# Optimization experiments

Hardware: AMD Instinct MI355X
Metric: run time of the kernel (lower is better)

The kernel has to match this reference:

```python
import jax, jax.numpy as jnp
import numpy as np
from jax import lax

TOP_K = 4
ROUTED_SCALING = 1.0
RENORMALIZE = True


def setup_inputs() -> dict:
    key = jax.random.key(0)
    ks = jax.random.split(key, 9)
    H, I, E = 2048, 1024, 16
    s = 0.02
    return {
        "hidden_states": jax.random.normal(ks[0], (2, 1024, H), jnp.float32),
        "gate_w": jax.random.normal(ks[1], (E, H), jnp.float32) * s,
        "expert_bias": jax.random.normal(ks[2], (E,), jnp.float32) * s,
        "w_gate": jax.random.normal(ks[3], (E, I, H), jnp.float32) * s,
        "w_up": jax.random.normal(ks[4], (E, I, H), jnp.float32) * s,
        "w_down": jax.random.normal(ks[5], (E, H, I), jnp.float32) * s,
        "sw_gate": jax.random.normal(ks[6], (I, H), jnp.float32) * s,
        "sw_up": jax.random.normal(ks[7], (I, H), jnp.float32) * s,
        "sw_down": jax.random.normal(ks[8], (H, I), jnp.float32) * s,
    }


def _swiglu_ffn(x, wg, wu, wd):
    # SiluAndMul(gate_up) -> down_proj
    return (jax.nn.silu(x @ wg.T) * (x @ wu.T)) @ wd.T


def reference(hidden_states, gate_w, expert_bias, w_gate, w_up, w_down,
              sw_gate, sw_up, sw_down):
    orig_shape = hidden_states.shape
    H = orig_shape[-1]
    x = hidden_states.reshape(-1, H)            # [T, H]
    T = x.shape[0]

    # --- sigmoid gating with score-correction bias (bias affects selection only) ---
    logits = x.astype(jnp.float32) @ gate_w.T    # [T, E] fp32 router
    scores = jax.nn.sigmoid(logits)
    _, topk_idx = lax.top_k(scores + expert_bias[None, :], TOP_K)   # [T, K]
    topk_w = jnp.take_along_axis(scores, topk_idx, axis=-1)         # raw scores
    if RENORMALIZE:
        topk_w = topk_w / jnp.sum(topk_w, axis=-1, keepdims=True)
    topk_w = topk_w * ROUTED_SCALING

    # scatter top-k weights into dense [T, E] combine matrix
    E = gate_w.shape[0]
    combine = jnp.zeros((T, E), dtype=x.dtype).at[
        jnp.arange(T)[:, None], topk_idx].set(topk_w.astype(x.dtype))

    # --- routed experts: scan over experts, weighted accumulate ---
    def step(acc, ws):
        wg, wu, wd, cw = ws                     # cw: [T] combine weights
        return acc + cw[:, None] * _swiglu_ffn(x, wg, wu, wd), None

    routed, _ = lax.scan(step, jnp.zeros_like(x),
                         (w_gate, w_up, w_down, combine.T))

    # --- shared expert ---
    shared = _swiglu_ffn(x, sw_gate, sw_up, sw_down)

    return (routed + shared).reshape(orig_shape)
```

## Files before the change

### kernel.cpp

```cpp
#include <hip/hip_runtime.h>
#include <hip/hip_bf16.h>
#include <cstdint>

#define TK 2048
#define HD 2048
#define ID 1024
#define NE 16
#define NG 17
#define TOPK 4
#define SLOTS (TK*TOPK)
#define ROWS_ALL (SLOTS+TK)
#define IH (ID*HD)
#define MAXT 96

typedef __attribute__((ext_vector_type(4))) float f32x4;
typedef __attribute__((ext_vector_type(8))) short s16x8;
typedef unsigned short u16;
typedef unsigned long long u64;

__device__ __forceinline__ u16 f2bf(float f){
  union { float f; uint32_t u; } v; v.f = f;
  uint32_t r = v.u + 0x7fffu + ((v.u >> 16) & 1u);
  return (u16)(r >> 16);
}

#define GLD16(g, l) __builtin_amdgcn_global_load_lds( \
    (const __attribute__((address_space(1))) void*)(g), \
    (__attribute__((address_space(3))) void*)(l), 16, 0, 0)

__device__ __forceinline__ const s16x8* fragp(const u16* b, int row, int off){
  return (const s16x8*)((const char*)b + row*128 + (off ^ ((row&7)<<4)));
}

__global__ void k_prep(const float* __restrict__ x, u16* __restrict__ xb,
                       float* __restrict__ out, int out_n, u64* __restrict__ maskbits){
  int gi = blockIdx.x*blockDim.x + threadIdx.x;
  int st = gridDim.x*blockDim.x;
  if (gi < NE*32) maskbits[gi] = 0ull;
  for (int i=gi; i<out_n; i+=st) out[i] = 0.f;
  for (int i=gi; i<TK*HD/4; i+=st){
    float4 f = ((const float4*)x)[i];
    ushort4 o; o.x=f2bf(f.x); o.y=f2bf(f.y); o.z=f2bf(f.z); o.w=f2bf(f.w);
    ((ushort4*)xb)[i] = o;
  }
}

__global__ void k_cvtw(const float* __restrict__ wg, const float* __restrict__ wu,
                       const float* __restrict__ wd, const float* __restrict__ swg,
                       const float* __restrict__ swu, const float* __restrict__ swd,
                       u16* __restrict__ wgb, u16* __restrict__ wub, u16* __restrict__ wdb){
  const size_t nbig = (size_t)NE*IH/4, nsml = IH/4;
  const size_t total = 3*nbig + 3*nsml;
  for (size_t i = (size_t)blockIdx.x*blockDim.x + threadIdx.x; i < total;
       i += (size_t)gridDim.x*blockDim.x){
    const float4* src; ushort4* dst; size_t j = i;
    if (j < nbig){ src=(const float4*)wg + j;  dst=(ushort4*)wgb + j; }
    else if ((j-=nbig) < nbig){ src=(const float4*)wu + j;  dst=(ushort4*)wub + j; }
    else if ((j-=nbig) < nbig){ src=(const float4*)wd + j;  dst=(ushort4*)wdb + j; }
    else if ((j-=nbig) < nsml){ src=(const float4*)swg + j; dst=(ushort4*)wgb + nbig + j; }
    else if ((j-=nsml) < nsml){ src=(const float4*)swu + j; dst=(ushort4*)wub + nbig + j; }
    else { j-=nsml; src=(const float4*)swd + j; dst=(ushort4*)wdb + nbig + j; }
    float4 f = *src;
    ushort4 o; o.x=f2bf(f.x); o.y=f2bf(f.y); o.z=f2bf(f.z); o.w=f2bf(f.w);
    *dst = o;
  }
}

__global__ __launch_bounds__(256) void k_logits(const float* __restrict__ x,
                                                const float* __restrict__ gw,
                                                const float* __restrict__ bias,
                                                float* __restrict__ wdense,
                                                u64* __restrict__ maskbits){
  int t = blockIdx.x, tid = threadIdx.x;
  int lane = tid & 63, wv = tid >> 6;
  const float* xr = x + (size_t)t*HD;
  float acc[NE];
  #pragma unroll
  for (int e=0;e<NE;e++) acc[e]=0.f;
  for (int k=tid;k<HD;k+=256){
    float xv = xr[k];
    #pragma unroll
    for (int e=0;e<NE;e++) acc[e] += xv * gw[e*HD + k];
  }
  __shared__ float red[NE][4];
  #pragma unroll
  for (int e=0;e<NE;e++){
    float v = acc[e];
    #pragma unroll
    for (int off=32;off>0;off>>=1) v += __shfl_down(v, off, 64);
    if (lane==0) red[e][wv] = v;
  }
  __syncthreads();
  if (tid == 0){
    float sc[NE], bs[NE];
    #pragma unroll
    for (int e=0;e<NE;e++){
      float l = red[e][0]+red[e][1]+red[e][2]+red[e][3];
      float s = 1.f/(1.f+expf(-l));
      sc[e]=s; bs[e]=s+bias[e];
    }
    int idx[TOPK]; float wsum=0.f; unsigned used=0;
    for (int k=0;k<TOPK;k++){
      int best=0; float bv=-1e30f;
      for (int e=0;e<NE;e++) if (!((used>>e)&1u) && bs[e] > bv){ bv=bs[e]; best=e; }
      used |= 1u<<best; idx[k]=best; wsum += sc[best];
    }
    float inv = 1.f/wsum;
    for (int k=0;k<TOPK;k++){
      int e = idx[k];
      wdense[t*NE + e] = sc[e]*inv;
      atomicOr(&maskbits[e*32 + (t>>6)], 1ull << (t&63));
    }
  }
}

__global__ void k_scan(const u64* __restrict__ maskbits, int* __restrict__ counts,
                       int* __restrict__ offsets, int* __restrict__ wordpfx,
                       int* __restrict__ tiles){
  int acc = 0;
  for (int e=0;e<NE;e++){
    int c = 0;
    for (int w=0;w<32;w++){ wordpfx[e*32+w] = c; c += __popcll(maskbits[e*32+w]); }
    counts[e] = c;
  }
  for (int e=0;e<NE;e++){ offsets[e] = acc; acc += counts[e]; }
  offsets[NE] = acc;
  counts[NE] = TK;
  int nt = 0;
  for (int g=0; g<NG; g++){
    int c = counts[g];
    for (int mt=0; mt*128 < c && nt < MAXT; mt++) tiles[nt++] = (g<<8) | mt;
  }
  for (; nt<MAXT; nt++) tiles[nt] = -1;
}

__global__ void k_scatter(const u64* __restrict__ maskbits, const int* __restrict__ offsets,
                          const int* __restrict__ wordpfx, const float* __restrict__ wdense,
                          int* __restrict__ rowtok, float* __restrict__ roww){
  int t = blockIdx.x*blockDim.x + threadIdx.x;
  int e = blockIdx.y;
  if (t >= TK) return;
  if (e == NE){ rowtok[offsets[NE]+t] = t; roww[offsets[NE]+t] = 1.f; return; }
  u64 w = maskbits[e*32 + (t>>6)];
  if ((w >> (t&63)) & 1ull){
    int pos = offsets[e] + wordpfx[e*32 + (t>>6)] + __popcll(w & ((1ull << (t&63)) - 1ull));
    rowtok[pos] = t; roww[pos] = wdense[t*NE + e];
  }
}

__global__ __launch_bounds__(256) void k_gemm1b(
    const u16* __restrict__ xb, const u16* __restrict__ wgb, const u16* __restrict__ wub,
    const int* __restrict__ counts, const int* __restrict__ offsets,
    const int* __restrict__ rowtok, const float* __restrict__ roww,
    const int* __restrict__ tiles, u16* __restrict__ P)
{
  int te = tiles[blockIdx.y];
  if (te < 0) return;
  int g = te >> 8, mt = te & 255;
  int cnt = counts[g];
  int n0 = blockIdx.x*64;
  int base = offsets[g];
  const u16* wg16 = wgb + (size_t)g*IH;
  const u16* wu16 = wub + (size_t)g*IH;

  __shared__ u16 lsA[128*64];
  __shared__ u16 lsG[64*64];
  __shared__ u16 lsU[64*64];

  int tid = threadIdx.x, lane = tid & 63, wv = tid >> 6;
  int wm = (wv>>1)*64, wn = (wv&1)*32;
  int rl = lane & 15, hi = lane >> 4;

  f32x4 accg[4][2] = {}; f32x4 accu[4][2] = {};

  const u16* aSrc[4];
  #pragma unroll
  for (int i=0;i<4;i++){
    int b = i*256 + tid, r = b>>3, cb = b&7;
    int m = mt*128 + r; if (m >= cnt) m = cnt-1;
    int tok = rowtok[base + m];
    aSrc[i] = xb + (size_t)tok*HD + ((cb ^ (r&7))<<3);
  }
  const u16 *gSrc[2], *uSrc[2];
  #pragma unroll
  for (int i=0;i<2;i++){
    int b = i*256 + tid, r = b>>3, cb = b&7;
    size_t off = (size_t)(n0 + r)*HD + ((cb ^ (r&7))<<3);
    gSrc[i] = wg16 + off; uSrc[i] = wu16 + off;
  }

  for (int k0=0; k0<HD; k0+=64){
    #pragma unroll
    for (int i=0;i<4;i++) GLD16(aSrc[i]+k0, lsA + (i*256 + wv*64)*8);
    #pragma unroll
    for (int i=0;i<2;i++) GLD16(gSrc[i]+k0, lsG + (i*256 + wv*64)*8);
    #pragma unroll
    for (int i=0;i<2;i++) GLD16(uSrc[i]+k0, lsU + (i*256 + wv*64)*8);
    __syncthreads();
    #pragma unroll
    for (int ks=0; ks<2; ++ks){
      int off = ks*64 + hi*16;
      s16x8 af[4];
      #pragma unroll
      for (int mi=0;mi<4;mi++) af[mi] = *fragp(lsA, wm+16*mi+rl, off);
      #pragma unroll
      for (int ni=0;ni<2;ni++){
        s16x8 bg = *fragp(lsG, wn+16*ni+rl, off);
        s16x8 bu = *fragp(lsU, wn+16*ni+rl, off);
        #pragma unroll
        for (int mi=0;mi<4;mi++){
          accg[mi][ni] = __builtin_amdgcn_mfma_f32_16x16x32_bf16(af[mi], bg, accg[mi][ni], 0,0,0);
          accu[mi][ni] = __builtin_amdgcn_mfma_f32_16x16x32_bf16(af[mi], bu, accu[mi][ni], 0,0,0);
        }
      }
    }
    __syncthreads();
  }
  int rl4 = hi*4, cl = rl;
  #pragma unroll
  for (int mi=0;mi<4;mi++){
    #pragma unroll
    for (int j=0;j<4;j++){
      int m = mt*128 + wm + mi*16 + rl4 + j;
      if (m < cnt){
        int slot = base + m;
        float wgt = roww[slot];
        #pragma unroll
        for (int ni=0;ni<2;ni++){
          float gv = accg[mi][ni][j], uv = accu[mi][ni][j];
          float pv = gv/(1.f+expf(-gv))*uv*wgt;
          P[(size_t)slot*ID + n0 + wn + ni*16 + cl] = f2bf(pv);
        }
      }
    }
  }
}

__global__ __launch_bounds__(256) void k_gemm2b(
    const u16* __restrict__ P, const u16* __restrict__ wdb,
    const int* __restrict__ counts, const int* __restrict__ offsets,
    const int* __restrict__ rowtok, const int* __restrict__ tiles,
    float* __restrict__ out)
{
  int te = tiles[blockIdx.y];
  if (te < 0) return;
  int g = te >> 8, mt = te & 255;
  int cnt = counts[g];
  int n0 = blockIdx.x*128;
  int base = offsets[g];
  const u16* wd16 = wdb + (size_t)g*IH;

  __shared__ u16 lsA[128*64];
  __shared__ u16 lsB[128*64];

  int tid = threadIdx.x, lane = tid & 63, wv = tid >> 6;
  int wm = (wv>>1)*64, wn = (wv&1)*64;
  int rl = lane & 15, hi = lane >> 4;
  f32x4 acc[4][4] = {};

  const u16 *aSrc[4], *bSrc[4];
  #pragma unroll
  for (int i=0;i<4;i++){
    int b = i*256 + tid, r = b>>3, cb = b&7;
    int m = mt*128 + r; if (m >= cnt) m = cnt-1;
    aSrc[i] = P + (size_t)(base + m)*ID + ((cb ^ (r&7))<<3);
    bSrc[i] = wd16 + (size_t)(n0 + r)*ID + ((cb ^ (r&7))<<3);
  }

  for (int k0=0; k0<ID; k0+=64){
    #pragma unroll
    for (int i=0;i<4;i++) GLD16(aSrc[i]+k0, lsA + (i*256 + wv*64)*8);
    #pragma unroll
    for (int i=0;i<4;i++) GLD16(bSrc[i]+k0, lsB + (i*256 + wv*64)*8);
    __syncthreads();
    #pragma unroll
    for (int ks=0; ks<2; ++ks){
      int off = ks*64 + hi*16;
      s16x8 af[4], bf[4];
      #pragma unroll
      for (int mi=0;mi<4;mi++) af[mi] = *fragp(lsA, wm+16*mi+rl, off);
      #pragma unroll
      for (int ni=0;ni<4;ni++) bf[ni] = *fragp(lsB, wn+16*ni+rl, off);
      #pragma unroll
      for (int mi=0;mi<4;mi++)
        #pragma unroll
        for (int ni=0;ni<4;ni++)
          acc[mi][ni] = __builtin_amdgcn_mfma_f32_16x16x32_bf16(af[mi], bf[ni], acc[mi][ni], 0,0,0);
    }
    __syncthreads();
  }
  int rl4 = hi*4, cl = rl;
  #pragma unroll
  for (int mi=0;mi<4;mi++){
    #pragma unroll
    for (int j=0;j<4;j++){
      int m = mt*128 + wm + mi*16 + rl4 + j;
      if (m < cnt){
        int tok = rowtok[base + m];
        #pragma unroll
        for (int ni=0;ni<4;ni++)
          atomicAdd(&out[(size_t)tok*HD + n0 + wn + ni*16 + cl], acc[mi][ni][j]);
      }
    }
  }
}

__global__ __launch_bounds__(256) void k_gemm1o(
    const u16* __restrict__ xb,
    const float* __restrict__ w_gate, const float* __restrict__ w_up,
    const float* __restrict__ sw_gate, const float* __restrict__ sw_up,
    const int* __restrict__ counts, const int* __restrict__ offsets,
    const int* __restrict__ rowtok, const float* __restrict__ roww,
    const int* __restrict__ tiles, u16* __restrict__ P)
{
  int te = tiles[blockIdx.y];
  if (te < 0) return;
  int g = te >> 8, mt = te & 255;
  int cnt = counts[g];
  int n0 = blockIdx.x*64;
  int base = offsets[g];
  const float* wg32 = (g<NE) ? w_gate + (size_t)g*IH : sw_gate;
  const float* wu32 = (g<NE) ? w_up   + (size_t)g*IH : sw_up;

  __shared__ u16 lsA[128][40];
  __shared__ u16 lsG[64][40];
  __shared__ u16 lsU[64][40];

  int tid = threadIdx.x, lane = tid & 63, wv = tid >> 6;
  int wm = (wv>>1)*64, wn = (wv&1)*32;
  f32x4 accg[4][2] = {}; f32x4 accu[4][2] = {};
  int arow = tid>>1, ahalf = tid&1;
  int am = mt*128 + arow;
  const u16* aptr = nullptr;
  if (am < cnt){ int tok = rowtok[base + am]; aptr = xb + (size_t)tok*HD + 16*ahalf; }

  for (int k0=0; k0<HD; k0+=32){
    uint4 a0 = {0,0,0,0}, a1 = {0,0,0,0};
    if (aptr){ a0 = *(const uint4*)(aptr + k0); a1 = *(const uint4*)(aptr + k0 + 8); }
    *(uint4*)&lsA[arow][16*ahalf]   = a0;
    *(uint4*)&lsA[arow][16*ahalf+8] = a1;
    int r = tid>>2, cg = tid&3;
    {
      const float* s = wg32 + (size_t)(n0+r)*HD + k0 + 8*cg;
      float4 f0 = *(const float4*)s, f1 = *(const float4*)(s+4);
      ushort4 o0, o1;
      o0.x=f2bf(f0.x); o0.y=f2bf(f0.y); o0.z=f2bf(f0.z); o0.w=f2bf(f0.w);
      o1.x=f2bf(f1.x); o1.y=f2bf(f1.y); o1.z=f2bf(f1.z); o1.w=f2bf(f1.w);
      *(ushort4*)&lsG[r][8*cg]   = o0;
      *(ushort4*)&lsG[r][8*cg+4] = o1;
    }
    {
      const float* s = wu32 + (size_t)(n0+r)*HD + k0 + 8*cg;
      float4 f0 = *(const float4*)s, f1 = *(const float4*)(s+4);
      ushort4 o0, o1;
      o0.x=f2bf(f0.x); o0.y=f2bf(f0.y); o0.z=f2bf(f0.z); o0.w=f2bf(f0.w);
      o1.x=f2bf(f1.x); o1.y=f2bf(f1.y); o1.z=f2bf(f1.z); o1.w=f2bf(f1.w);
      *(ushort4*)&lsU[r][8*cg]   = o0;
      *(ushort4*)&lsU[r][8*cg+4] = o1;
    }
    __syncthreads();
    int kb = 8*(lane>>4), rl = lane&15;
    s16x8 af[4];
    #pragma unroll
    for (int mi=0;mi<4;mi++) af[mi] = *(const s16x8*)&lsA[wm+16*mi+rl][kb];
    #pragma unroll
    for (int ni=0;ni<2;ni++){
      s16x8 bg = *(const s16x8*)&lsG[wn+16*ni+rl][kb];
      s16x8 bu = *(const s16x8*)&lsU[wn+16*ni+rl][kb];
      #pragma unroll
      for (int mi=0;mi<4;mi++){
        accg[mi][ni] = __builtin_amdgcn_mfma_f32_16x16x32_bf16(af[mi], bg, accg[mi][ni], 0,0,0);
        accu[mi][ni] = __builtin_amdgcn_mfma_f32_16x16x32_bf16(af[mi], bu, accu[mi][ni], 0,0,0);
      }
    }
    __syncthreads();
  }
  int rl4 = (lane>>4)*4, cl = lane&15;
  #pragma unroll
  for (int mi=0;mi<4;mi++){
    #pragma unroll
    for (int j=0;j<4;j++){
      int m = mt*128 + wm + mi*16 + rl4 + j;
      if (m < cnt){
        int slot = base + m;
        float wgt = roww[slot];
        #pragma unroll
        for (int ni=0;ni<2;ni++){
          float gv = accg[mi][ni][j], uv = accu[mi][ni][j];
          float pv = gv/(1.f+expf(-gv))*uv*wgt;
          P[(size_t)slot*ID + n0 + wn + ni*16 + cl] = f2bf(pv);
        }
      }
    }
  }
}

__global__ __launch_bounds__(256) void k_gemm2o(
    const u16* __restrict__ P,
    const float* __restrict__ w_down, const float* __restrict__ sw_down,
    const int* __restrict__ counts, const int* __restrict__ offsets,
    const int* __restrict__ rowtok, const int* __restrict__ tiles,
    float* __restrict__ out)
{
  int te = tiles[blockIdx.y];
  if (te < 0) return;
  int g = te >> 8, mt = te & 255;
  int cnt = counts[g];
  int n0 = blockIdx.x*128;
  int base = offsets[g];
  const float* wd32 = (g<NE) ? w_down + (size_t)g*IH : sw_down;

  __shared__ u16 lsA[128][40];
  __shared__ u16 lsB[128][40];

  int tid = threadIdx.x, lane = tid & 63, wv = tid >> 6;
  int wm = (wv>>1)*64, wn = (wv&1)*64;
  f32x4 acc[4][4] = {};
  int arow = tid>>1, ahalf = tid&1;
  int am = mt*128 + arow;
  const u16* aptr = (am < cnt) ? P + (size_t)(base+am)*ID + 16*ahalf : nullptr;

  for (int k0=0; k0<ID; k0+=32){
    uint4 a0 = {0,0,0,0}, a1 = {0,0,0,0};
    if (aptr){ a0 = *(const uint4*)(aptr + k0); a1 = *(const uint4*)(aptr + k0 + 8); }
    *(uint4*)&lsA[arow][16*ahalf]   = a0;
    *(uint4*)&lsA[arow][16*ahalf+8] = a1;
    int r = tid>>1, hf = tid&1;
    const float* s = wd32 + (size_t)(n0+r)*ID + k0 + 16*hf;
    float4 f0=*(const float4*)s, f1=*(const float4*)(s+4), f2=*(const float4*)(s+8), f3=*(const float4*)(s+12);
    ushort4 o0,o1,o2,o3;
    o0.x=f2bf(f0.x); o0.y=f2bf(f0.y); o0.z=f2bf(f0.z); o0.w=f2bf(f0.w);
    o1.x=f2bf(f1.x); o1.y=f2bf(f1.y); o1.z=f2bf(f1.z); o1.w=f2bf(f1.w);
    o2.x=f2bf(f2.x); o2.y=f2bf(f2.y); o2.z=f2bf(f2.z); o2.w=f2bf(f2.w);
    o3.x=f2bf(f3.x); o3.y=f2bf(f3.y); o3.z=f2bf(f3.z); o3.w=f2bf(f3.w);
    *(ushort4*)&lsB[r][16*hf]    = o0;
    *(ushort4*)&lsB[r][16*hf+4]  = o1;
    *(ushort4*)&lsB[r][16*hf+8]  = o2;
    *(ushort4*)&lsB[r][16*hf+12] = o3;
    __syncthreads();
    int kb = 8*(lane>>4), rl = lane&15;
    s16x8 af[4], bfr[4];
    #pragma unroll
    for (int mi=0;mi<4;mi++) af[mi]  = *(const s16x8*)&lsA[wm+16*mi+rl][kb];
    #pragma unroll
    for (int ni=0;ni<4;ni++) bfr[ni] = *(const s16x8*)&lsB[wn+16*ni+rl][kb];
    #pragma unroll
    for (int mi=0;mi<4;mi++)
      #pragma unroll
      for (int ni=0;ni<4;ni++)
        acc[mi][ni] = __builtin_amdgcn_mfma_f32_16x16x32_bf16(af[mi], bfr[ni], acc[mi][ni], 0,0,0);
    __syncthreads();
  }
  int rl4 = (lane>>4)*4, cl = lane&15;
  #pragma unroll
  for (int mi=0;mi<4;mi++){
    #pragma unroll
    for (int j=0;j<4;j++){
      int m = mt*128 + wm + mi*16 + rl4 + j;
      if (m < cnt){
        int tok = rowtok[base + m];
        #pragma unroll
        for (int ni=0;ni<4;ni++)
          atomicAdd(&out[(size_t)tok*HD + n0 + wn + ni*16 + cl], acc[mi][ni][j]);
      }
    }
  }
}


extern "C" void kernel_launch(void* const* d_in, const int* in_sizes, int n_in,
                              void* d_out, int out_size, void* d_ws, size_t ws_size,
                              hipStream_t stream){
  (void)in_sizes; (void)n_in;
  const float* x       = (const float*)d_in[0];
  const float* gate_w  = (const float*)d_in[1];
  const float* ebias   = (const float*)d_in[2];
  const float* w_gate  = (const float*)d_in[3];
  const float* w_up    = (const float*)d_in[4];
  const float* w_down  = (const float*)d_in[5];
  const float* sw_gate = (const float*)d_in[6];
  const float* sw_up   = (const float*)d_in[7];
  const float* sw_down = (const float*)d_in[8];
  float* out = (float*)d_out;

  char* p = (char*)d_ws;
  auto alloc = [&](size_t bytes)->char*{ char* r = p; p += (bytes + 255) & ~(size_t)255; return r; };
  u16*   xb       = (u16*)  alloc((size_t)TK*HD*2);
  u16*   P        = (u16*)  alloc((size_t)ROWS_ALL*ID*2);
  float* wdense   = (float*)alloc((size_t)TK*NE*4);
  u64*   maskbits = (u64*)  alloc((size_t)NE*32*8);
  int*   wordpfx  = (int*)  alloc((size_t)NE*32*4);
  int*   counts   = (int*)  alloc(64);
  int*   offsets  = (int*)  alloc(64);
  int*   tiles    = (int*)  alloc(MAXT*4);
  int*   rowtok   = (int*)  alloc((size_t)ROWS_ALL*4);
  float* roww     = (float*)alloc((size_t)ROWS_ALL*4);
  size_t base_end = (size_t)(p - (char*)d_ws);
  size_t slab = (size_t)NG*IH*2;
  bool big = ws_size >= base_end + 3*slab + 4096;
  u16 *wgb=nullptr, *wub=nullptr, *wdb=nullptr;
  if (big){ wgb=(u16*)alloc(slab); wub=(u16*)alloc(slab); wdb=(u16*)alloc(slab); }

  k_prep<<<2048, 256, 0, stream>>>(x, xb, out, out_size, maskbits);
  if (big)
    k_cvtw<<<2048, 256, 0, stream>>>(w_gate, w_up, w_down, sw_gate, sw_up, sw_down,
                                     wgb, wub, wdb);
  k_logits<<<TK, 256, 0, stream>>>(x, gate_w, ebias, wdense, maskbits);
  k_scan<<<1, 1, 0, stream>>>(maskbits, counts, offsets, wordpfx, tiles);
  k_scatter<<<dim3(TK/256, NG), 256, 0, stream>>>(maskbits, offsets, wordpfx, wdense, rowtok, roww);

  dim3 g1(ID/64, MAXT);
  dim3 g2(HD/128, MAXT);
  if (big){
    k_gemm1b<<<g1, 256, 0, stream>>>(xb, wgb, wub, counts, offsets, rowtok, roww, tiles, P);
    k_gemm2b<<<g2, 256, 0, stream>>>(P, wdb, counts, offsets, rowtok, tiles, out);
  } else {
    k_gemm1o<<<g1, 256, 0, stream>>>(xb, w_gate, w_up, sw_gate, sw_up,
                                     counts, offsets, rowtok, roww, tiles, P);
    k_gemm2o<<<g2, 256, 0, stream>>>(P, w_down, sw_down, counts, offsets, rowtok, tiles, out);
  }
}
```

Baseline: 428.9 us.

## Convert expert weights on the fly in double-buffered GEMMs, drop bf16 weight pre-pass

Removes the separate pass that converted all expert weights to bf16 in workspace. The grouped GEMMs now read fp32 weights directly, convert them in registers and store them into swizzled, double-buffered LDS, while activations are prefetched with async global-to-LDS loads. This avoids writing and rereading a large bf16 weight copy each call. In exchange, each tile rereads fp32 weights, doubling weight bytes per tile load, and uses more LDS and registers.

```diff
diff --git a/kernel.cpp b/kernel.cpp
--- a/kernel.cpp
+++ b/kernel.cpp
@@ -24,6 +24,13 @@
   return (u16)(r >> 16);
 }
 
+__device__ __forceinline__ uint4 pack8(float4 a, float4 b){
+  u16 h[8];
+  h[0]=f2bf(a.x); h[1]=f2bf(a.y); h[2]=f2bf(a.z); h[3]=f2bf(a.w);
+  h[4]=f2bf(b.x); h[5]=f2bf(b.y); h[6]=f2bf(b.z); h[7]=f2bf(b.w);
+  return *(uint4*)h;
+}
+
 #define GLD16(g, l) __builtin_amdgcn_global_load_lds( \
     (const __attribute__((address_space(1))) void*)(g), \
     (__attribute__((address_space(3))) void*)(l), 16, 0, 0)
@@ -42,27 +49,6 @@
     float4 f = ((const float4*)x)[i];
     ushort4 o; o.x=f2bf(f.x); o.y=f2bf(f.y); o.z=f2bf(f.z); o.w=f2bf(f.w);
     ((ushort4*)xb)[i] = o;
-  }
-}
-
-__global__ void k_cvtw(const float* __restrict__ wg, const float* __restrict__ wu,
-                       const float* __restrict__ wd, const float* __restrict__ swg,
-                       const float* __restrict__ swu, const float* __restrict__ swd,
-                       u16* __restrict__ wgb, u16* __restrict__ wub, u16* __restrict__ wdb){
-  const size_t nbig = (size_t)NE*IH/4, nsml = IH/4;
-  const size_t total = 3*nbig + 3*nsml;
-  for (size_t i = (size_t)blockIdx.x*blockDim.x + threadIdx.x; i < total;
-       i += (size_t)gridDim.x*blockDim.x){
-    const float4* src; ushort4* dst; size_t j = i;
-    if (j < nbig){ src=(const float4*)wg + j;  dst=(ushort4*)wgb + j; }
-    else if ((j-=nbig) < nbig){ src=(const float4*)wu + j;  dst=(ushort4*)wub + j; }
-    else if ((j-=nbig) < nbig){ src=(const float4*)wd + j;  dst=(ushort4*)wdb + j; }
-    else if ((j-=nbig) < nsml){ src=(const float4*)swg + j; dst=(ushort4*)wgb + nbig + j; }
-    else if ((j-=nsml) < nsml){ src=(const float4*)swu + j; dst=(ushort4*)wub + nbig + j; }
-    else { j-=nsml; src=(const float4*)swd + j; dst=(ushort4*)wdb + nbig + j; }
-    float4 f = *src;
-    ushort4 o; o.x=f2bf(f.x); o.y=f2bf(f.y); o.z=f2bf(f.z); o.w=f2bf(f.w);
-    *dst = o;
   }
 }
 
@@ -148,164 +134,7 @@
   }
 }
 
-__global__ __launch_bounds__(256) void k_gemm1b(
-    const u16* __restrict__ xb, const u16* __restrict__ wgb, const u16* __restrict__ wub,
-    const int* __restrict__ counts, const int* __restrict__ offsets,
-    const int* __restrict__ rowtok, const float* __restrict__ roww,
-    const int* __restrict__ tiles, u16* __restrict__ P)
-{
-  int te = tiles[blockIdx.y];
-  if (te < 0) return;
-  int g = te >> 8, mt = te & 255;
-  int cnt = counts[g];
-  int n0 = blockIdx.x*64;
-  int base = offsets[g];
-  const u16* wg16 = wgb + (size_t)g*IH;
-  const u16* wu16 = wub + (size_t)g*IH;
-
-  __shared__ u16 lsA[128*64];
-  __shared__ u16 lsG[64*64];
-  __shared__ u16 lsU[64*64];
-
-  int tid = threadIdx.x, lane = tid & 63, wv = tid >> 6;
-  int wm = (wv>>1)*64, wn = (wv&1)*32;
-  int rl = lane & 15, hi = lane >> 4;
-
-  f32x4 accg[4][2] = {}; f32x4 accu[4][2] = {};
-
-  const u16* aSrc[4];
-  #pragma unroll
-  for (int i=0;i<4;i++){
-    int b = i*256 + tid, r = b>>3, cb = b&7;
-    int m = mt*128 + r; if (m >= cnt) m = cnt-1;
-    int tok = rowtok[base + m];
-    aSrc[i] = xb + (size_t)tok*HD + ((cb ^ (r&7))<<3);
-  }
-  const u16 *gSrc[2], *uSrc[2];
-  #pragma unroll
-  for (int i=0;i<2;i++){
-    int b = i*256 + tid, r = b>>3, cb = b&7;
-    size_t off = (size_t)(n0 + r)*HD + ((cb ^ (r&7))<<3);
-    gSrc[i] = wg16 + off; uSrc[i] = wu16 + off;
-  }
-
-  for (int k0=0; k0<HD; k0+=64){
-    #pragma unroll
-    for (int i=0;i<4;i++) GLD16(aSrc[i]+k0, lsA + (i*256 + wv*64)*8);
-    #pragma unroll
-    for (int i=0;i<2;i++) GLD16(gSrc[i]+k0, lsG + (i*256 + wv*64)*8);
-    #pragma unroll
-    for (int i=0;i<2;i++) GLD16(uSrc[i]+k0, lsU + (i*256 + wv*64)*8);
-    __syncthreads();
-    #pragma unroll
-    for (int ks=0; ks<2; ++ks){
-      int off = ks*64 + hi*16;
-      s16x8 af[4];
-      #pragma unroll
-      for (int mi=0;mi<4;mi++) af[mi] = *fragp(lsA, wm+16*mi+rl, off);
-      #pragma unroll
-      for (int ni=0;ni<2;ni++){
-        s16x8 bg = *fragp(lsG, wn+16*ni+rl, off);
-        s16x8 bu = *fragp(lsU, wn+16*ni+rl, off);
-        #pragma unroll
-        for (int mi=0;mi<4;mi++){
-          accg[mi][ni] = __builtin_amdgcn_mfma_f32_16x16x32_bf16(af[mi], bg, accg[mi][ni], 0,0,0);
-          accu[mi][ni] = __builtin_amdgcn_mfma_f32_16x16x32_bf16(af[mi], bu, accu[mi][ni], 0,0,0);
-        }
-      }
-    }
-    __syncthreads();
-  }
-  int rl4 = hi*4, cl = rl;
-  #pragma unroll
-  for (int mi=0;mi<4;mi++){
-    #pragma unroll
-    for (int j=0;j<4;j++){
-      int m = mt*128 + wm + mi*16 + rl4 + j;
-      if (m < cnt){
-        int slot = base + m;
-        float wgt = roww[slot];
-        #pragma unroll
-        for (int ni=0;ni<2;ni++){
-          float gv = accg[mi][ni][j], uv = accu[mi][ni][j];
-          float pv = gv/(1.f+expf(-gv))*uv*wgt;
-          P[(size_t)slot*ID + n0 + wn + ni*16 + cl] = f2bf(pv);
-        }
-      }
-    }
-  }
-}
-
-__global__ __launch_bounds__(256) void k_gemm2b(
-    const u16* __restrict__ P, const u16* __restrict__ wdb,
-    const int* __restrict__ counts, const int* __restrict__ offsets,
-    const int* __restrict__ rowtok, const int* __restrict__ tiles,
-    float* __restrict__ out)
-{
-  int te = tiles[blockIdx.y];
-  if (te < 0) return;
-  int g = te >> 8, mt = te & 255;
-  int cnt = counts[g];
-  int n0 = blockIdx.x*128;
-  int base = offsets[g];
-  const u16* wd16 = wdb + (size_t)g*IH;
-
-  __shared__ u16 lsA[128*64];
-  __shared__ u16 lsB[128*64];
-
-  int tid = threadIdx.x, lane = tid & 63, wv = tid >> 6;
-  int wm = (wv>>1)*64, wn = (wv&1)*64;
-  int rl = lane & 15, hi = lane >> 4;
-  f32x4 acc[4][4] = {};
-
-  const u16 *aSrc[4], *bSrc[4];
-  #pragma unroll
-  for (int i=0;i<4;i++){
-    int b = i*256 + tid, r = b>>3, cb = b&7;
-    int m = mt*128 + r; if (m >= cnt) m = cnt-1;
-    aSrc[i] = P + (size_t)(base + m)*ID + ((cb ^ (r&7))<<3);
-    bSrc[i] = wd16 + (size_t)(n0 + r)*ID + ((cb ^ (r&7))<<3);
-  }
-
-  for (int k0=0; k0<ID; k0+=64){
-    #pragma unroll
-    for (int i=0;i<4;i++) GLD16(aSrc[i]+k0, lsA + (i*256 + wv*64)*8);
-    #pragma unroll
-    for (int i=0;i<4;i++) GLD16(bSrc[i]+k0, lsB + (i*256 + wv*64)*8);
-    __syncthreads();
-    #pragma unroll
-    for (int ks=0; ks<2; ++ks){
-      int off = ks*64 + hi*16;
-      s16x8 af[4], bf[4];
-      #pragma unroll
-      for (int mi=0;mi<4;mi++) af[mi] = *fragp(lsA, wm+16*mi+rl, off);
-      #pragma unroll
-      for (int ni=0;ni<4;ni++) bf[ni] = *fragp(lsB, wn+16*ni+rl, off);
-      #pragma unroll
-      for (int mi=0;mi<4;mi++)
-        #pragma unroll
-        for (int ni=0;ni<4;ni++)
-          acc[mi][ni] = __builtin_amdgcn_mfma_f32_16x16x32_bf16(af[mi], bf[ni], acc[mi][ni], 0,0,0);
-    }
-    __syncthreads();
-  }
-  int rl4 = hi*4, cl = rl;
-  #pragma unroll
-  for (int mi=0;mi<4;mi++){
-    #pragma unroll
-    for (int j=0;j<4;j++){
-      int m = mt*128 + wm + mi*16 + rl4 + j;
-      if (m < cnt){
-        int tok = rowtok[base + m];
-        #pragma unroll
-        for (int ni=0;ni<4;ni++)
-          atomicAdd(&out[(size_t)tok*HD + n0 + wn + ni*16 + cl], acc[mi][ni][j]);
-      }
-    }
-  }
-}
-
-__global__ __launch_bounds__(256) void k_gemm1o(
+__global__ __launch_bounds__(256) void k_gemm1(
     const u16* __restrict__ xb,
     const float* __restrict__ w_gate, const float* __restrict__ w_up,
     const float* __restrict__ sw_gate, const float* __restrict__ sw_up,
@@ -322,60 +151,87 @@
   const float* wg32 = (g<NE) ? w_gate + (size_t)g*IH : sw_gate;
   const float* wu32 = (g<NE) ? w_up   + (size_t)g*IH : sw_up;
 
-  __shared__ u16 lsA[128][40];
-  __shared__ u16 lsG[64][40];
-  __shared__ u16 lsU[64][40];
+  __shared__ u16 lsA[2][128*64];
+  __shared__ u16 lsG[2][64*64];
+  __shared__ u16 lsU[2][64*64];
 
   int tid = threadIdx.x, lane = tid & 63, wv = tid >> 6;
   int wm = (wv>>1)*64, wn = (wv&1)*32;
+  int rl = lane & 15, hi = lane >> 4;
+
   f32x4 accg[4][2] = {}; f32x4 accu[4][2] = {};
-  int arow = tid>>1, ahalf = tid&1;
-  int am = mt*128 + arow;
-  const u16* aptr = nullptr;
-  if (am < cnt){ int tok = rowtok[base + am]; aptr = xb + (size_t)tok*HD + 16*ahalf; }
-
-  for (int k0=0; k0<HD; k0+=32){
-    uint4 a0 = {0,0,0,0}, a1 = {0,0,0,0};
-    if (aptr){ a0 = *(const uint4*)(aptr + k0); a1 = *(const uint4*)(aptr + k0 + 8); }
-    *(uint4*)&lsA[arow][16*ahalf]   = a0;
-    *(uint4*)&lsA[arow][16*ahalf+8] = a1;
-    int r = tid>>2, cg = tid&3;
-    {
-      const float* s = wg32 + (size_t)(n0+r)*HD + k0 + 8*cg;
-      float4 f0 = *(const float4*)s, f1 = *(const float4*)(s+4);
-      ushort4 o0, o1;
-      o0.x=f2bf(f0.x); o0.y=f2bf(f0.y); o0.z=f2bf(f0.z); o0.w=f2bf(f0.w);
-      o1.x=f2bf(f1.x); o1.y=f2bf(f1.y); o1.z=f2bf(f1.z); o1.w=f2bf(f1.w);
-      *(ushort4*)&lsG[r][8*cg]   = o0;
-      *(ushort4*)&lsG[r][8*cg+4] = o1;
-    }
-    {
-      const float* s = wu32 + (size_t)(n0+r)*HD + k0 + 8*cg;
-      float4 f0 = *(const float4*)s, f1 = *(const float4*)(s+4);
-      ushort4 o0, o1;
-      o0.x=f2bf(f0.x); o0.y=f2bf(f0.y); o0.z=f2bf(f0.z); o0.w=f2bf(f0.w);
-      o1.x=f2bf(f1.x); o1.y=f2bf(f1.y); o1.z=f2bf(f1.z); o1.w=f2bf(f1.w);
-      *(ushort4*)&lsU[r][8*cg]   = o0;
-      *(ushort4*)&lsU[r][8*cg+4] = o1;
+
+  const u16* aSrc[4];
+  #pragma unroll
+  for (int i=0;i<4;i++){
+    int b = i*256 + tid, r = b>>3, cb = b&7;
+    int m = mt*128 + r; if (m >= cnt) m = cnt-1;
+    int tok = rowtok[base + m];
+    aSrc[i] = xb + (size_t)tok*HD + ((cb ^ (r&7))<<3);
+  }
+  int wrow = tid>>2, wq = tid&3;
+  const float* gW = wg32 + (size_t)(n0+wrow)*HD + wq*16;
+  const float* uW = wu32 + (size_t)(n0+wrow)*HD + wq*16;
+  int wb0 = (wrow*128 + wq*32) ^ ((wrow&7)<<4);
+  char* gBase = (char*)&lsG[0][0];
+  char* uBase = (char*)&lsU[0][0];
+
+  float4 gr[4], ur[4];
+  #pragma unroll
+  for (int j=0;j<4;j++){ gr[j] = ((const float4*)gW)[j]; ur[j] = ((const float4*)uW)[j]; }
+  #pragma unroll
+  for (int i=0;i<4;i++) GLD16(aSrc[i], &lsA[0][(i*256 + wv*64)*8]);
+  {
+    uint4 g0 = pack8(gr[0],gr[1]), g1 = pack8(gr[2],gr[3]);
+    uint4 u0 = pack8(ur[0],ur[1]), u1 = pack8(ur[2],ur[3]);
+    *(uint4*)(gBase + wb0)      = g0;
+    *(uint4*)(gBase + (wb0^16)) = g1;
+    *(uint4*)(uBase + wb0)      = u0;
+    *(uint4*)(uBase + (wb0^16)) = u1;
+  }
+  __syncthreads();
+
+  const int ntile = HD/64;
+  for (int t=0; t<ntile; ++t){
+    int cur = t & 1, nxt = cur ^ 1;
+    bool more = (t+1 < ntile);
+    int k1 = (t+1)*64;
+    if (more){
+      #pragma unroll
+      for (int j=0;j<4;j++){ gr[j] = ((const float4*)(gW+k1))[j]; ur[j] = ((const float4*)(uW+k1))[j]; }
+      #pragma unroll
+      for (int i=0;i<4;i++) GLD16(aSrc[i]+k1, &lsA[nxt][(i*256 + wv*64)*8]);
+    }
+    const u16* A = lsA[cur]; const u16* G = lsG[cur]; const u16* U = lsU[cur];
+    #pragma unroll
+    for (int ks=0; ks<2; ++ks){
+      int off = ks*64 + hi*16;
+      s16x8 af[4];
+      #pragma unroll
+      for (int mi=0;mi<4;mi++) af[mi] = *fragp(A, wm+16*mi+rl, off);
+      #pragma unroll
+      for (int ni=0;ni<2;ni++){
+        s16x8 bg = *fragp(G, wn+16*ni+rl, off);
+        s16x8 bu = *fragp(U, wn+16*ni+rl, off);
+        #pragma unroll
+        for (int mi=0;mi<4;mi++){
+          accg[mi][ni] = __builtin_amdgcn_mfma_f32_16x16x32_bf16(af[mi], bg, accg[mi][ni], 0,0,0);
+          accu[mi][ni] = __builtin_amdgcn_mfma_f32_16x16x32_bf16(af[mi], bu, accu[mi][ni], 0,0,0);
+        }
+      }
+    }
+    if (more){
+      uint4 g0 = pack8(gr[0],gr[1]), g1 = pack8(gr[2],gr[3]);
+      uint4 u0 = pack8(ur[0],ur[1]), u1 = pack8(ur[2],ur[3]);
+      char* gd = gBase + nxt*8192; char* ud = uBase + nxt*8192;
+      *(uint4*)(gd + wb0)      = g0;
+      *(uint4*)(gd + (wb0^16)) = g1;
+      *(uint4*)(ud + wb0)      = u0;
+      *(uint4*)(ud + (wb0^16)) = u1;
     }
     __syncthreads();
-    int kb = 8*(lane>>4), rl = lane&15;
-    s16x8 af[4];
-    #pragma unroll
-    for (int mi=0;mi<4;mi++) af[mi] = *(const s16x8*)&lsA[wm+16*mi+rl][kb];
-    #pragma unroll
-    for (int ni=0;ni<2;ni++){
-      s16x8 bg = *(const s16x8*)&lsG[wn+16*ni+rl][kb];
-      s16x8 bu = *(const s16x8*)&lsU[wn+16*ni+rl][kb];
-      #pragma unroll
-      for (int mi=0;mi<4;mi++){
-        accg[mi][ni] = __builtin_amdgcn_mfma_f32_16x16x32_bf16(af[mi], bg, accg[mi][ni], 0,0,0);
-        accu[mi][ni] = __builtin_amdgcn_mfma_f32_16x16x32_bf16(af[mi], bu, accu[mi][ni], 0,0,0);
-      }
-    }
-    __syncthreads();
-  }
-  int rl4 = (lane>>4)*4, cl = lane&15;
+  }
+  int rl4 = hi*4, cl = rl;
   #pragma unroll
   for (int mi=0;mi<4;mi++){
     #pragma unroll
@@ -395,7 +251,7 @@
   }
 }
 
-__global__ __launch_bounds__(256) void k_gemm2o(
+__global__ __launch_bounds__(256) void k_gemm2(
     const u16* __restrict__ P,
     const float* __restrict__ w_down, const float* __restrict__ sw_down,
     const int* __restrict__ counts, const int* __restrict__ offsets,
@@ -410,48 +266,77 @@
   int base = offsets[g];
   const float* wd32 = (g<NE) ? w_down + (size_t)g*IH : sw_down;
 
-  __shared__ u16 lsA[128][40];
-  __shared__ u16 lsB[128][40];
+  __shared__ u16 lsA[2][128*64];
+  __shared__ u16 lsB[2][128*64];
 
   int tid = threadIdx.x, lane = tid & 63, wv = tid >> 6;
   int wm = (wv>>1)*64, wn = (wv&1)*64;
+  int rl = lane & 15, hi = lane >> 4;
   f32x4 acc[4][4] = {};
-  int arow = tid>>1, ahalf = tid&1;
-  int am = mt*128 + arow;
-  const u16* aptr = (am < cnt) ? P + (size_t)(base+am)*ID + 16*ahalf : nullptr;
-
-  for (int k0=0; k0<ID; k0+=32){
-    uint4 a0 = {0,0,0,0}, a1 = {0,0,0,0};
-    if (aptr){ a0 = *(const uint4*)(aptr + k0); a1 = *(const uint4*)(aptr + k0 + 8); }
-    *(uint4*)&lsA[arow][16*ahalf]   = a0;
-    *(uint4*)&lsA[arow][16*ahalf+8] = a1;
-    int r = tid>>1, hf = tid&1;
-    const float* s = wd32 + (size_t)(n0+r)*ID + k0 + 16*hf;
-    float4 f0=*(const float4*)s, f1=*(const float4*)(s+4), f2=*(const float4*)(s+8), f3=*(const float4*)(s+12);
-    ushort4 o0,o1,o2,o3;
-    o0.x=f2bf(f0.x); o0.y=f2bf(f0.y); o0.z=f2bf(f0.z); o0.w=f2bf(f0.w);
-    o1.x=f2bf(f1.x); o1.y=f2bf(f1.y); o1.z=f2bf(f1.z); o1.w=f2bf(f1.w);
-    o2.x=f2bf(f2.x); o2.y=f2bf(f2.y); o2.z=f2bf(f2.z); o2.w=f2bf(f2.w);
-    o3.x=f2bf(f3.x); o3.y=f2bf(f3.y); o3.z=f2bf(f3.z); o3.w=f2bf(f3.w);
-    *(ushort4*)&lsB[r][16*hf]    = o0;
-    *(ushort4*)&lsB[r][16*hf+4]  = o1;
-    *(ushort4*)&lsB[r][16*hf+8]  = o2;
-    *(ushort4*)&lsB[r][16*hf+12] = o3;
+
+  const u16* aSrc[4];
+  #pragma unroll
+  for (int i=0;i<4;i++){
+    int b = i*256 + tid, r = b>>3, cb = b&7;
+    int m = mt*128 + r; if (m >= cnt) m = cnt-1;
+    aSrc[i] = P + (size_t)(base + m)*ID + ((cb ^ (r&7))<<3);
+  }
+  int brow = tid>>1, bh = tid&1;
+  const float* bW = wd32 + (size_t)(n0+brow)*ID + bh*32;
+  int bb = (brow*128 + bh*64) ^ ((brow&7)<<4);
+  char* bBase = (char*)&lsB[0][0];
+
+  float4 br[8];
+  #pragma unroll
+  for (int j=0;j<8;j++) br[j] = ((const float4*)bW)[j];
+  #pragma unroll
+  for (int i=0;i<4;i++) GLD16(aSrc[i], &lsA[0][(i*256 + wv*64)*8]);
+  {
+    #pragma unroll
+    for (int c=0;c<4;c++){
+      uint4 w = pack8(br[2*c], br[2*c+1]);
+      *(uint4*)(bBase + (bb ^ (c*16))) = w;
+    }
+  }
+  __syncthreads();
+
+  const int ntile = ID/64;
+  for (int t=0; t<ntile; ++t){
+    int cur = t & 1, nxt = cur ^ 1;
+    bool more = (t+1 < ntile);
+    int k1 = (t+1)*64;
+    if (more){
+      #pragma unroll
+      for (int j=0;j<8;j++) br[j] = ((const float4*)(bW+k1))[j];
+      #pragma unroll
+      for (int i=0;i<4;i++) GLD16(aSrc[i]+k1, &lsA[nxt][(i*256 + wv*64)*8]);
+    }
+    const u16* A = lsA[cur]; const u16* B = lsB[cur];
+    #pragma unroll
+    for (int ks=0; ks<2; ++ks){
+      int off = ks*64 + hi*16;
+      s16x8 af[4], bf[4];
+      #pragma unroll
+      for (int mi=0;mi<4;mi++) af[mi] = *fragp(A, wm+16*mi+rl, off);
+      #pragma unroll
+      for (int ni=0;ni<4;ni++) bf[ni] = *fragp(B, wn+16*ni+rl, off);
+      #pragma unroll
+      for (int mi=0;mi<4;mi++)
+        #pragma unroll
+        for (int ni=0;ni<4;ni++)
+          acc[mi][ni] = __builtin_amdgcn_mfma_f32_16x16x32_bf16(af[mi], bf[ni], acc[mi][ni], 0,0,0);
+    }
+    if (more){
+      char* bd = bBase + nxt*16384;
+      #pragma unroll
+      for (int c=0;c<4;c++){
+        uint4 w = pack8(br[2*c], br[2*c+1]);
+        *(uint4*)(bd + (bb ^ (c*16))) = w;
+      }
+    }
     __syncthreads();
-    int kb = 8*(lane>>4), rl = lane&15;
-    s16x8 af[4], bfr[4];
-    #pragma unroll
-    for (int mi=0;mi<4;mi++) af[mi]  = *(const s16x8*)&lsA[wm+16*mi+rl][kb];
-    #pragma unroll
-    for (int ni=0;ni<4;ni++) bfr[ni] = *(const s16x8*)&lsB[wn+16*ni+rl][kb];
-    #pragma unroll
-    for (int mi=0;mi<4;mi++)
-      #pragma unroll
-      for (int ni=0;ni<4;ni++)
-        acc[mi][ni] = __builtin_amdgcn_mfma_f32_16x16x32_bf16(af[mi], bfr[ni], acc[mi][ni], 0,0,0);
-    __syncthreads();
-  }
-  int rl4 = (lane>>4)*4, cl = lane&15;
+  }
+  int rl4 = hi*4, cl = rl;
   #pragma unroll
   for (int mi=0;mi<4;mi++){
     #pragma unroll
@@ -471,7 +356,7 @@
 extern "C" void kernel_launch(void* const* d_in, const int* in_sizes, int n_in,
                               void* d_out, int out_size, void* d_ws, size_t ws_size,
                               hipStream_t stream){
-  (void)in_sizes; (void)n_in;
+  (void)in_sizes; (void)n_in; (void)ws_size;
   const float* x       = (const float*)d_in[0];
   const float* gate_w  = (const float*)d_in[1];
   const float* ebias   = (const float*)d_in[2];
@@ -495,28 +380,15 @@
   int*   tiles    = (int*)  alloc(MAXT*4);
   int*   rowtok   = (int*)  alloc((size_t)ROWS_ALL*4);
   float* roww     = (float*)alloc((size_t)ROWS_ALL*4);
-  size_t base_end = (size_t)(p - (char*)d_ws);
-  size_t slab = (size_t)NG*IH*2;
-  bool big = ws_size >= base_end + 3*slab + 4096;
-  u16 *wgb=nullptr, *wub=nullptr, *wdb=nullptr;
-  if (big){ wgb=(u16*)alloc(slab); wub=(u16*)alloc(slab); wdb=(u16*)alloc(slab); }
 
   k_prep<<<2048, 256, 0, stream>>>(x, xb, out, out_size, maskbits);
-  if (big)
-    k_cvtw<<<2048, 256, 0, stream>>>(w_gate, w_up, w_down, sw_gate, sw_up, sw_down,
-                                     wgb, wub, wdb);
   k_logits<<<TK, 256, 0, stream>>>(x, gate_w, ebias, wdense, maskbits);
   k_scan<<<1, 1, 0, stream>>>(maskbits, counts, offsets, wordpfx, tiles);
   k_scatter<<<dim3(TK/256, NG), 256, 0, stream>>>(maskbits, offsets, wordpfx, wdense, rowtok, roww);
 
   dim3 g1(ID/64, MAXT);
   dim3 g2(HD/128, MAXT);
-  if (big){
-    k_gemm1b<<<g1, 256, 0, stream>>>(xb, wgb, wub, counts, offsets, rowtok, roww, tiles, P);
-    k_gemm2b<<<g2, 256, 0, stream>>>(P, wdb, counts, offsets, rowtok, tiles, out);
-  } else {
-    k_gemm1o<<<g1, 256, 0, stream>>>(xb, w_gate, w_up, sw_gate, sw_up,
-                                     counts, offsets, rowtok, roww, tiles, P);
-    k_gemm2o<<<g2, 256, 0, stream>>>(P, w_down, sw_down, counts, offsets, rowtok, tiles, out);
-  }
-}
+  k_gemm1<<<g1, 256, 0, stream>>>(xb, w_gate, w_up, sw_gate, sw_up,
+                                  counts, offsets, rowtok, roww, tiles, P);
+  k_gemm2<<<g2, 256, 0, stream>>>(P, w_down, sw_down, counts, offsets, rowtok, tiles, out);
+}
```

Measured after the change: 489.7 us. 14.2% more time.
